# Kernel tuning notes

Hardware: AMD Instinct MI355X
Metric: run time of the kernel (lower is better)

## Reference

```python
import jax, jax.numpy as jnp
import numpy as np

DIM = 384
HEADS = 6
HEAD_DIM = DIM // HEADS
HIDDEN = 4 * DIM
EPS = 1e-5


def layer_norm(x, w, b):
    m = jnp.mean(x, axis=-1, keepdims=True)
    v = jnp.mean((x - m) ** 2, axis=-1, keepdims=True)
    return (x - m) * jax.lax.rsqrt(v + EPS) * w + b


def setup_inputs() -> dict:
    key = jax.random.key(0)
    ks = jax.random.split(key, 8)
    B, N = 2, 4096
    s_in = 1.0 / np.sqrt(DIM)
    s_h = 1.0 / np.sqrt(HIDDEN)
    return {
        "x": jax.random.normal(ks[0], (B, N, DIM), dtype=jnp.float32),
        "qkv_w": jax.random.normal(ks[1], (3 * DIM, DIM), dtype=jnp.float32) * s_in,
        "proj_w": jax.random.normal(ks[2], (DIM, DIM), dtype=jnp.float32) * s_in,
        "proj_b": jnp.zeros((DIM,), dtype=jnp.float32),
        "ln1_w": jnp.ones((DIM,), dtype=jnp.float32),
        "ln1_b": jnp.zeros((DIM,), dtype=jnp.float32),
        "ln2_w": jnp.ones((DIM,), dtype=jnp.float32),
        "ln2_b": jnp.zeros((DIM,), dtype=jnp.float32),
        "fc1_w": jax.random.normal(ks[3], (HIDDEN, DIM), dtype=jnp.float32) * s_in,
        "fc1_b": jnp.zeros((HIDDEN,), dtype=jnp.float32),
        "fc2_w": jax.random.normal(ks[4], (DIM, HIDDEN), dtype=jnp.float32) * s_h,
        "fc2_b": jnp.zeros((DIM,), dtype=jnp.float32),
    }


def reference(x, qkv_w, proj_w, proj_b, ln1_w, ln1_b, ln2_w, ln2_b,
              fc1_w, fc1_b, fc2_w, fc2_b):
    B, N, C = x.shape
    scale = HEAD_DIM ** (-0.5)

    # pre-norm attention
    y = layer_norm(x, ln1_w, ln1_b)
    qkv = (y @ qkv_w.T).reshape(B, N, 3, HEADS, HEAD_DIM)
    qkv = jnp.transpose(qkv, (2, 0, 3, 1, 4))  # [3, B, H, N, D]
    q, k, v = qkv[0], qkv[1], qkv[2]
    attn = jnp.einsum("bhnd,bhmd->bhnm", q, k) * scale  # [B,H,N,N]
    attn = jax.nn.softmax(attn, axis=-1)
    y = jnp.einsum("bhnm,bhmd->bhnd", attn, v)
    y = jnp.transpose(y, (0, 2, 1, 3)).reshape(B, N, C)
    y = y @ proj_w.T + proj_b

    # residual + LN2 + MLP (faithful to source: output = 2 * mlp(ln2(x + y)))
    x = x + y
    x = layer_norm(x, ln2_w, ln2_b)
    h = jax.nn.gelu(x @ fc1_w.T + fc1_b, approximate=False)
    x = h @ fc2_w.T + fc2_b
    x = x + x
    return x
```

## Files before the change

### kernel.cpp

```cpp
#include <hip/hip_runtime.h>
#include <hip/hip_bf16.h>

#define DIM 384
#define HEADS 6
#define HD 64
#define HIDDEN 1536
#define SEQ 4096
#define BATCH 2
#define NTOK (BATCH*SEQ)
#define QKVN (3*DIM)

typedef __attribute__((ext_vector_type(4))) float f32x4;
typedef __attribute__((ext_vector_type(16))) float f32x16;
typedef __attribute__((ext_vector_type(8))) short s16x8;
typedef __attribute__((ext_vector_type(4))) unsigned int u32x4;

__device__ __forceinline__ ushort f2bf(float f) {
    union { float f; unsigned u; } v; v.f = f;
    unsigned r = v.u + 0x7FFF + ((v.u >> 16) & 1);
    return (ushort)(r >> 16);
}
__device__ __forceinline__ float bf2f(ushort b) {
    union { unsigned u; float f; } v; v.u = ((unsigned)b) << 16;
    return v.f;
}
__device__ __forceinline__ unsigned cvtpk(float lo, float hi) {
    unsigned r;
    asm("v_cvt_pk_bf16_f32 %0, %1, %2" : "=v"(r) : "v"(lo), "v"(hi));
    return r;
}
__device__ __forceinline__ void pl32swap(unsigned& a, unsigned& b) {
    asm volatile("v_permlane32_swap_b32 %0, %1" : "+v"(a), "+v"(b));
}
__device__ __forceinline__ void g2l(const ushort* g, ushort* s) {
    __builtin_amdgcn_global_load_lds((const __attribute__((address_space(1))) void*)g,
                                     (__attribute__((address_space(3))) void*)s, 16, 0, 0);
}
__device__ __forceinline__ void blockbar() {
    asm volatile("" ::: "memory");
    __builtin_amdgcn_s_barrier();
    asm volatile("" ::: "memory");
}

__global__ void cvt4_kernel(const float4* __restrict__ s0, ushort* __restrict__ d0, int n0,
                            const float4* __restrict__ s1, ushort* __restrict__ d1, int n1,
                            const float4* __restrict__ s2, ushort* __restrict__ d2, int n2,
                            const float4* __restrict__ s3, ushort* __restrict__ d3, int n3) {
    int i = blockIdx.x * 256 + threadIdx.x;
    const float4* s; ushort* d; int k = i;
    if (i < n0) { s = s0; d = d0; }
    else { k -= n0; if (k < n1) { s = s1; d = d1; }
        else { k -= n1; if (k < n2) { s = s2; d = d2; }
            else { k -= n2; if (k >= n3) return; s = s3; d = d3; } } }
    float4 v = s[k];
    ushort4 o; o.x = f2bf(v.x); o.y = f2bf(v.y); o.z = f2bf(v.z); o.w = f2bf(v.w);
    *(ushort4*)(d + (size_t)k * 4) = o;
}

__global__ __launch_bounds__(256) void ln_kernel(const float* __restrict__ x,
        const float* __restrict__ w, const float* __restrict__ b,
        ushort* __restrict__ y) {
    int l = threadIdx.x & 63;
    int row = blockIdx.x * 4 + (threadIdx.x >> 6);
    const float* xr = x + (size_t)row * DIM;
    float v[6], s = 0.f, s2 = 0.f;
#pragma unroll
    for (int i = 0; i < 6; ++i) { v[i] = xr[l + 64*i]; s += v[i]; s2 += v[i]*v[i]; }
#pragma unroll
    for (int d = 1; d < 64; d <<= 1) { s += __shfl_xor(s, d); s2 += __shfl_xor(s2, d); }
    float mean = s * (1.f/DIM);
    float var  = s2 * (1.f/DIM) - mean*mean;
    float rstd = rsqrtf(var + 1e-5f);
    ushort* yr = y + (size_t)row * DIM;
#pragma unroll
    for (int i = 0; i < 6; ++i) {
        int c = l + 64*i;
        yr[c] = f2bf((v[i]-mean)*rstd*w[c] + b[c]);
    }
}

template<int EPI, int BN>
__global__ __launch_bounds__(256, (BN == 128 ? 3 : 4)) void gemm_kernel(
        const ushort* __restrict__ A, const ushort* __restrict__ W,
        const float* __restrict__ bias, const float* __restrict__ resid,
        void* __restrict__ Cout, int M, int N, int K) {
    __shared__ __align__(16) ushort lds_a[2][64*64];
    __shared__ __align__(16) ushort lds_w[2][BN*64];
    const int t = threadIdx.x, l = t & 63, wid = t >> 6;
    const int lo = l & 15, lg = l >> 4;
    const int m0 = blockIdx.x * 64, n0 = blockIdx.y * BN;
    constexpr int NI = BN / 32;
    constexpr int WW = BN / 32;
    const int wm = (wid & 1) * 32, wn = (wid >> 1) * (BN / 2);
    f32x4 acc[2][NI] = {};

    const int srow8 = l >> 3;
    const int schunk = (l & 7) ^ srow8;
    const ushort* gA[2];
#pragma unroll
    for (int w = 0; w < 2; ++w)
        gA[w] = A + (size_t)(m0 + wid*16 + w*8 + srow8) * K + schunk*8;
    const ushort* gW[WW];
#pragma unroll
    for (int w = 0; w < WW; ++w)
        gW[w] = W + (size_t)(n0 + wid*(8*WW) + w*8 + srow8) * K + schunk*8;

#define STAGE(BUF, K0) do {                                                    \
    _Pragma("unroll")                                                          \
    for (int w = 0; w < 2; ++w)  g2l(gA[w] + (K0), &lds_a[BUF][(wid*16 + w*8)*64]); \
    _Pragma("unroll")                                                          \
    for (int w = 0; w < WW; ++w) g2l(gW[w] + (K0), &lds_w[BUF][(wid*(8*WW) + w*8)*64]); \
} while (0)

#define WAITC do {                                                             \
    if constexpr (BN == 128) asm volatile("s_waitcnt vmcnt(6)" ::: "memory");  \
    else                     asm volatile("s_waitcnt vmcnt(4)" ::: "memory");  \
} while (0)
#define WAIT0 asm volatile("s_waitcnt vmcnt(0)" ::: "memory")

    const int lo7 = lo & 7;
#define COMPUTE(BUF) do {                                                      \
    _Pragma("unroll")                                                          \
    for (int kk = 0; kk < 2; ++kk) {                                           \
        const int ch = ((kk*4 + lg) ^ lo7) * 8;                                \
        s16x8 af[2], bfr[NI];                                                  \
        _Pragma("unroll")                                                      \
        for (int mi = 0; mi < 2; ++mi)                                         \
            af[mi] = *(const s16x8*)&lds_a[BUF][(wm + mi*16 + lo)*64 + ch];    \
        _Pragma("unroll")                                                      \
        for (int ni = 0; ni < NI; ++ni)                                        \
            bfr[ni] = *(const s16x8*)&lds_w[BUF][(wn + ni*16 + lo)*64 + ch];   \
        _Pragma("unroll")                                                      \
        for (int mi = 0; mi < 2; ++mi)                                         \
            _Pragma("unroll")                                                  \
            for (int ni = 0; ni < NI; ++ni)                                    \
                acc[mi][ni] = __builtin_amdgcn_mfma_f32_16x16x32_bf16(af[mi], bfr[ni], acc[mi][ni], 0,0,0); \
    }                                                                          \
} while (0)

    STAGE(0, 0);
    int k0 = 0, remaining = K / 64;
    while (true) {
        if (remaining > 1) { STAGE(1, k0 + 64); WAITC; } else WAIT0;
        blockbar();
        COMPUTE(0);
        blockbar();
        k0 += 64; if (--remaining == 0) break;
        if (remaining > 1) { STAGE(0, k0 + 64); WAITC; } else WAIT0;
        blockbar();
        COMPUTE(1);
        blockbar();
        k0 += 64; if (--remaining == 0) break;
    }
#undef STAGE
#undef WAITC
#undef WAIT0
#undef COMPUTE

#pragma unroll
    for (int mi = 0; mi < 2; ++mi)
#pragma unroll
    for (int ni = 0; ni < NI; ++ni)
#pragma unroll
    for (int r = 0; r < 4; ++r) {
        int row = m0 + wm + mi*16 + lg*4 + r;
        int col = n0 + wn + ni*16 + lo;
        float c = acc[mi][ni][r];
        size_t idx = (size_t)row * N + col;
        if (EPI == 0) {
            ((ushort*)Cout)[idx] = f2bf(c);
        } else if (EPI == 1) {
            ((float*)Cout)[idx] = c + bias[col] + resid[idx];
        } else if (EPI == 2) {
            c += bias[col];
            ((ushort*)Cout)[idx] = f2bf(0.5f * c * (1.f + erff(c * 0.70710678118f)));
        } else {
            ((float*)Cout)[idx] = 2.f * (c + bias[col]);
        }
    }
}

#define PV_STEP(S, MM, CB) do {                                                   \
    unsigned w0 = cvtpk(S[8*MM+0], S[8*MM+1]);                                    \
    unsigned w1 = cvtpk(S[8*MM+2], S[8*MM+3]);                                    \
    unsigned w2 = cvtpk(S[8*MM+4], S[8*MM+5]);                                    \
    unsigned w3 = cvtpk(S[8*MM+6], S[8*MM+7]);                                    \
    pl32swap(w0, w2); pl32swap(w1, w3);                                           \
    u32x4 fw = {w0, w1, w2, w3};                                                  \
    s16x8 pa = __builtin_bit_cast(s16x8, fw);                                     \
    int colb = ((CB) + G*8) ^ swz0;                                               \
    s16x8 vb0 = *(const s16x8*)&lds_v[half][q31][colb];                           \
    s16x8 vb1 = *(const s16x8*)&lds_v[half][32 + q31][colb ^ 32];                 \
    o0 = __builtin_amdgcn_mfma_f32_32x32x16_bf16(pa, vb0, o0, 0,0,0);             \
    o1 = __builtin_amdgcn_mfma_f32_32x32x16_bf16(pa, vb1, o1, 0,0,0);             \
    ol = __builtin_amdgcn_mfma_f32_32x32x16_bf16(pa, vones, ol, 0,0,0);           \
} while (0)

__global__ __launch_bounds__(256, 3) void attn_kernel(const ushort* __restrict__ qkv,
                                                      ushort* __restrict__ out) {
    __shared__ __align__(16) ushort lds_k[2][64][72];
    __shared__ __align__(16) ushort lds_v[2][64][72];
    const int t = threadIdx.x, l = t & 63, wid = t >> 6;
    const int G = l >> 5, q31 = l & 31, half = wid >> 1;
    const int b = blockIdx.y / HEADS, h = blockIdx.y % HEADS;
    const ushort* base = qkv + (size_t)b * SEQ * QKVN + h * HD;
    const int q0 = blockIdx.x * 64 + (wid & 1) * 32;

    const float QSC = 0.1803368801111137f;
    s16x8 qf[4];
#pragma unroll
    for (int dc = 0; dc < 4; ++dc) {
        s16x8 qv = *(const s16x8*)(base + (size_t)(q0 + q31) * QKVN + dc*16 + G*8);
#pragma unroll
        for (int j = 0; j < 8; ++j)
            qv[j] = (short)f2bf(bf2f((ushort)qv[j]) * QSC);
        qf[dc] = qv;
    }
    s16x8 vones;
#pragma unroll
    for (int j = 0; j < 8; ++j) vones[j] = (short)0x3F80;

    f32x16 o0 = {}, o1 = {}, ol = {};

    const int u = t & 127, sa = u >> 3, sc = u & 7;
    const ushort* kbase = base + DIM;
    const ushort* vbase = base + 2*DIM;
    const int key0base = half * (SEQ/2);
    const int swz0 = ((q31 >> 3) & 3) << 3;

    s16x8 kreg[4], vreg[4];
#pragma unroll
    for (int p = 0; p < 4; ++p) {
        kreg[p] = *(const s16x8*)(kbase + (size_t)(key0base + p*16 + sa) * QKVN + sc*8);
        vreg[p] = *(const s16x8*)(vbase + (size_t)(key0base + p*16 + sa) * QKVN + sc*8);
    }

    for (int it = 0; it < 32; ++it) {
        const int key0 = key0base + it*64;
        __syncthreads();
#pragma unroll
        for (int p = 0; p < 4; ++p) {
            *(s16x8*)&lds_k[half][p*16 + sa][sc*8] = kreg[p];
            const int colp = (p*16 + sa) ^ ((sc & 3) << 3) ^ ((sc >> 2) << 5);
#pragma unroll
            for (int j = 0; j < 8; ++j)
                lds_v[half][sc*8 + j][colp] = (ushort)vreg[p][j];
        }
        __syncthreads();
        if (it < 31) {
#pragma unroll
            for (int p = 0; p < 4; ++p) {
                kreg[p] = *(const s16x8*)(kbase + (size_t)(key0 + 64 + p*16 + sa) * QKVN + sc*8);
                vreg[p] = *(const s16x8*)(vbase + (size_t)(key0 + 64 + p*16 + sa) * QKVN + sc*8);
            }
        }

        f32x16 st0 = {}, st1 = {};
        __builtin_amdgcn_s_setprio(1);
#pragma unroll
        for (int dc = 0; dc < 4; ++dc) {
            s16x8 kf0 = *(const s16x8*)&lds_k[half][q31][dc*16 + G*8];
            s16x8 kf1 = *(const s16x8*)&lds_k[half][32 + q31][dc*16 + G*8];
            st0 = __builtin_amdgcn_mfma_f32_32x32x16_bf16(kf0, qf[dc], st0, 0,0,0);
            st1 = __builtin_amdgcn_mfma_f32_32x32x16_bf16(kf1, qf[dc], st1, 0,0,0);
        }
        __builtin_amdgcn_s_setprio(0);

#pragma unroll
        for (int r = 0; r < 16; ++r) {
            st0[r] = exp2f(st0[r]);
            st1[r] = exp2f(st1[r]);
        }

        __builtin_amdgcn_s_setprio(1);
        PV_STEP(st0, 0, 0);
        PV_STEP(st0, 1, 16);
        PV_STEP(st1, 0, 32);
        PV_STEP(st1, 1, 48);
        __builtin_amdgcn_s_setprio(0);
    }

    __syncthreads();
    float* mb = (float*)&lds_k[0][0][0];
    float* ml = (float*)&lds_v[0][0][0];
    if (half == 1) {
#pragma unroll
        for (int r = 0; r < 16; ++r) {
            mb[((wid&1)*2 + 0)*1024 + r*64 + l] = o0[r];
            mb[((wid&1)*2 + 1)*1024 + r*64 + l] = o1[r];
            ml[(wid&1)*1024 + r*64 + l] = ol[r];
        }
    }
    __syncthreads();
    if (half == 0) {
        ushort* ob = out + (size_t)b * SEQ * DIM + h * HD;
#pragma unroll
        for (int r = 0; r < 16; ++r) {
            float invr = 1.0f / (ol[r] + ml[(wid&1)*1024 + r*64 + l]);
            float v0 = (o0[r] + mb[((wid&1)*2 + 0)*1024 + r*64 + l]) * invr;
            float v1 = (o1[r] + mb[((wid&1)*2 + 1)*1024 + r*64 + l]) * invr;
            int qr = (r & 3) + 8*(r >> 2) + 4*G;
            int row = q0 + qr;
            ob[(size_t)row * DIM + q31]      = f2bf(v0);
            ob[(size_t)row * DIM + 32 + q31] = f2bf(v1);
        }
    }
}

extern "C" void kernel_launch(void* const* d_in, const int* in_sizes, int n_in,
                              void* d_out, int out_size, void* d_ws, size_t ws_size,
                              hipStream_t stream) {
    const float* x      = (const float*)d_in[0];
    const float* qkv_w  = (const float*)d_in[1];
    const float* proj_w = (const float*)d_in[2];
    const float* proj_b = (const float*)d_in[3];
    const float* ln1_w  = (const float*)d_in[4];
    const float* ln1_b  = (const float*)d_in[5];
    const float* ln2_w  = (const float*)d_in[6];
    const float* ln2_b  = (const float*)d_in[7];
    const float* fc1_w  = (const float*)d_in[8];
    const float* fc1_b  = (const float*)d_in[9];
    const float* fc2_w  = (const float*)d_in[10];
    const float* fc2_b  = (const float*)d_in[11];
    float* outp = (float*)d_out;

    char* ws = (char*)d_ws;
    size_t off = 0;
    auto alloc = [&](size_t bytes) {
        off = (off + 255) & ~(size_t)255;
        void* p = ws + off;
        off += bytes;
        return p;
    };
    ushort* wq   = (ushort*)alloc((size_t)QKVN * DIM * 2);
    ushort* wp   = (ushort*)alloc((size_t)DIM * DIM * 2);
    ushort* w1   = (ushort*)alloc((size_t)HIDDEN * DIM * 2);
    ushort* w2   = (ushort*)alloc((size_t)DIM * HIDDEN * 2);
    ushort* y1   = (ushort*)alloc((size_t)NTOK * DIM * 2);
    ushort* qkvb = (ushort*)alloc((size_t)NTOK * QKVN * 2);
    ushort* ao   = (ushort*)alloc((size_t)NTOK * DIM * 2);
    float*  res  = (float*) alloc((size_t)NTOK * DIM * 4);
    ushort* y2   = (ushort*)alloc((size_t)NTOK * DIM * 2);
    ushort* hb   = (ushort*)alloc((size_t)NTOK * HIDDEN * 2);

    const int n0 = QKVN*DIM/4, n1 = DIM*DIM/4, n2 = HIDDEN*DIM/4, n3 = DIM*HIDDEN/4;
    cvt4_kernel<<<(n0+n1+n2+n3 + 255)/256, 256, 0, stream>>>(
        (const float4*)qkv_w, wq, n0, (const float4*)proj_w, wp, n1,
        (const float4*)fc1_w, w1, n2, (const float4*)fc2_w, w2, n3);

    ln_kernel<<<NTOK/4, 256, 0, stream>>>(x, ln1_w, ln1_b, y1);
    gemm_kernel<0,128><<<dim3(NTOK/64, QKVN/128), 256, 0, stream>>>(y1, wq, nullptr, nullptr, qkvb, NTOK, QKVN, DIM);
    attn_kernel<<<dim3(SEQ/64, BATCH*HEADS), 256, 0, stream>>>(qkvb, ao);
    gemm_kernel<1,64><<<dim3(NTOK/64, DIM/64), 256, 0, stream>>>(ao, wp, proj_b, x, res, NTOK, DIM, DIM);
    ln_kernel<<<NTOK/4, 256, 0, stream>>>(res, ln2_w, ln2_b, y2);
    gemm_kernel<2,128><<<dim3(NTOK/64, HIDDEN/128), 256, 0, stream>>>(y2, w1, fc1_b, nullptr, hb, NTOK, HIDDEN, DIM);
    gemm_kernel<3,64><<<dim3(NTOK/64, DIM/64), 256, 0, stream>>>(hb, w2, fc2_b, nullptr, outp, NTOK, DIM, HIDDEN);
}
```

Measured before the change: 248.7 us.

## Pre-transpose V in a separate kernel and merge weight cast with LN1

```diff
diff --git a/kernel.cpp b/kernel.cpp
--- a/kernel.cpp
+++ b/kernel.cpp
@@ -42,19 +42,44 @@
     asm volatile("" ::: "memory");
 }
 
-__global__ void cvt4_kernel(const float4* __restrict__ s0, ushort* __restrict__ d0, int n0,
-                            const float4* __restrict__ s1, ushort* __restrict__ d1, int n1,
-                            const float4* __restrict__ s2, ushort* __restrict__ d2, int n2,
-                            const float4* __restrict__ s3, ushort* __restrict__ d3, int n3) {
-    int i = blockIdx.x * 256 + threadIdx.x;
-    const float4* s; ushort* d; int k = i;
-    if (i < n0) { s = s0; d = d0; }
-    else { k -= n0; if (k < n1) { s = s1; d = d1; }
-        else { k -= n1; if (k < n2) { s = s2; d = d2; }
-            else { k -= n2; if (k >= n3) return; s = s3; d = d3; } } }
-    float4 v = s[k];
-    ushort4 o; o.x = f2bf(v.x); o.y = f2bf(v.y); o.z = f2bf(v.z); o.w = f2bf(v.w);
-    *(ushort4*)(d + (size_t)k * 4) = o;
+__global__ __launch_bounds__(256) void prep_kernel(
+        const float4* __restrict__ s0, ushort* __restrict__ d0, int n0,
+        const float4* __restrict__ s1, ushort* __restrict__ d1, int n1,
+        const float4* __restrict__ s2, ushort* __restrict__ d2, int n2,
+        const float4* __restrict__ s3, ushort* __restrict__ d3, int n3,
+        int ncvt,
+        const float* __restrict__ x, const float* __restrict__ lw,
+        const float* __restrict__ lb, ushort* __restrict__ y) {
+    const int bx = blockIdx.x, t = threadIdx.x;
+    if (bx < ncvt) {
+        int i = bx * 256 + t;
+        const float4* s; ushort* d; int k = i;
+        if (i < n0) { s = s0; d = d0; }
+        else { k -= n0; if (k < n1) { s = s1; d = d1; }
+            else { k -= n1; if (k < n2) { s = s2; d = d2; }
+                else { k -= n2; if (k >= n3) return; s = s3; d = d3; } } }
+        float4 v = s[k];
+        ushort4 o; o.x = f2bf(v.x); o.y = f2bf(v.y); o.z = f2bf(v.z); o.w = f2bf(v.w);
+        *(ushort4*)(d + (size_t)k * 4) = o;
+    } else {
+        int l = t & 63;
+        int row = (bx - ncvt) * 4 + (t >> 6);
+        const float* xr = x + (size_t)row * DIM;
+        float v[6], s = 0.f, s2 = 0.f;
+#pragma unroll
+        for (int i = 0; i < 6; ++i) { v[i] = xr[l + 64*i]; s += v[i]; s2 += v[i]*v[i]; }
+#pragma unroll
+        for (int d = 1; d < 64; d <<= 1) { s += __shfl_xor(s, d); s2 += __shfl_xor(s2, d); }
+        float mean = s * (1.f/DIM);
+        float var  = s2 * (1.f/DIM) - mean*mean;
+        float rstd = rsqrtf(var + 1e-5f);
+        ushort* yr = y + (size_t)row * DIM;
+#pragma unroll
+        for (int i = 0; i < 6; ++i) {
+            int c = l + 64*i;
+            yr[c] = f2bf((v[i]-mean)*rstd*lw[c] + lb[c]);
+        }
+    }
 }
 
 __global__ __launch_bounds__(256) void ln_kernel(const float* __restrict__ x,
@@ -76,6 +101,32 @@
     for (int i = 0; i < 6; ++i) {
         int c = l + 64*i;
         yr[c] = f2bf((v[i]-mean)*rstd*w[c] + b[c]);
+    }
+}
+
+__global__ __launch_bounds__(256) void vtrans_kernel(const ushort* __restrict__ qkvb,
+                                                     ushort* __restrict__ vt) {
+    __shared__ __align__(16) ushort lds[64][72];
+    const int t = threadIdx.x;
+    const int key0 = blockIdx.x * 64;
+    const int bh = blockIdx.y;
+    const int b = bh / HEADS, h = bh % HEADS;
+    const ushort* src = qkvb + (size_t)b * SEQ * QKVN + 2*DIM + h*HD;
+    const int ky = t >> 3, c = t & 7;
+#pragma unroll
+    for (int hf = 0; hf < 2; ++hf) {
+        s16x8 v = *(const s16x8*)(src + (size_t)(key0 + hf*32 + ky) * QKVN + c*8);
+        *(s16x8*)&lds[hf*32 + ky][c*8] = v;
+    }
+    __syncthreads();
+    ushort* dst = vt + (size_t)bh * 64 * SEQ + key0;
+#pragma unroll
+    for (int hf = 0; hf < 2; ++hf) {
+        const int d = hf*32 + (t >> 3), kc = t & 7;
+        s16x8 o;
+#pragma unroll
+        for (int j = 0; j < 8; ++j) o[j] = (short)lds[kc*8 + j][d];
+        *(s16x8*)(dst + (size_t)d * SEQ + kc*8) = o;
     }
 }
 
@@ -188,15 +239,16 @@
     pl32swap(w0, w2); pl32swap(w1, w3);                                           \
     u32x4 fw = {w0, w1, w2, w3};                                                  \
     s16x8 pa = __builtin_bit_cast(s16x8, fw);                                     \
-    int colb = ((CB) + G*8) ^ swz0;                                               \
+    int colb = (CB) + G*8;                                                        \
     s16x8 vb0 = *(const s16x8*)&lds_v[half][q31][colb];                           \
-    s16x8 vb1 = *(const s16x8*)&lds_v[half][32 + q31][colb ^ 32];                 \
+    s16x8 vb1 = *(const s16x8*)&lds_v[half][32 + q31][colb];                      \
     o0 = __builtin_amdgcn_mfma_f32_32x32x16_bf16(pa, vb0, o0, 0,0,0);             \
     o1 = __builtin_amdgcn_mfma_f32_32x32x16_bf16(pa, vb1, o1, 0,0,0);             \
     ol = __builtin_amdgcn_mfma_f32_32x32x16_bf16(pa, vones, ol, 0,0,0);           \
 } while (0)
 
 __global__ __launch_bounds__(256, 3) void attn_kernel(const ushort* __restrict__ qkv,
+                                                      const ushort* __restrict__ vt,
                                                       ushort* __restrict__ out) {
     __shared__ __align__(16) ushort lds_k[2][64][72];
     __shared__ __align__(16) ushort lds_v[2][64][72];
@@ -204,6 +256,7 @@
     const int G = l >> 5, q31 = l & 31, half = wid >> 1;
     const int b = blockIdx.y / HEADS, h = blockIdx.y % HEADS;
     const ushort* base = qkv + (size_t)b * SEQ * QKVN + h * HD;
+    const ushort* vtb = vt + (size_t)blockIdx.y * 64 * SEQ;
     const int q0 = blockIdx.x * 64 + (wid & 1) * 32;
 
     const float QSC = 0.1803368801111137f;
@@ -224,15 +277,13 @@
 
     const int u = t & 127, sa = u >> 3, sc = u & 7;
     const ushort* kbase = base + DIM;
-    const ushort* vbase = base + 2*DIM;
     const int key0base = half * (SEQ/2);
-    const int swz0 = ((q31 >> 3) & 3) << 3;
 
     s16x8 kreg[4], vreg[4];
 #pragma unroll
     for (int p = 0; p < 4; ++p) {
         kreg[p] = *(const s16x8*)(kbase + (size_t)(key0base + p*16 + sa) * QKVN + sc*8);
-        vreg[p] = *(const s16x8*)(vbase + (size_t)(key0base + p*16 + sa) * QKVN + sc*8);
+        vreg[p] = *(const s16x8*)(vtb + (size_t)(sa + p*16) * SEQ + key0base + sc*8);
     }
 
     for (int it = 0; it < 32; ++it) {
@@ -241,17 +292,14 @@
 #pragma unroll
         for (int p = 0; p < 4; ++p) {
             *(s16x8*)&lds_k[half][p*16 + sa][sc*8] = kreg[p];
-            const int colp = (p*16 + sa) ^ ((sc & 3) << 3) ^ ((sc >> 2) << 5);
-#pragma unroll
-            for (int j = 0; j < 8; ++j)
-                lds_v[half][sc*8 + j][colp] = (ushort)vreg[p][j];
+            *(s16x8*)&lds_v[half][sa + p*16][sc*8] = vreg[p];
         }
         __syncthreads();
         if (it < 31) {
 #pragma unroll
             for (int p = 0; p < 4; ++p) {
                 kreg[p] = *(const s16x8*)(kbase + (size_t)(key0 + 64 + p*16 + sa) * QKVN + sc*8);
-                vreg[p] = *(const s16x8*)(vbase + (size_t)(key0 + 64 + p*16 + sa) * QKVN + sc*8);
+                vreg[p] = *(const s16x8*)(vtb + (size_t)(sa + p*16) * SEQ + key0 + 64 + sc*8);
             }
         }
 
@@ -338,19 +386,22 @@
     ushort* w2   = (ushort*)alloc((size_t)DIM * HIDDEN * 2);
     ushort* y1   = (ushort*)alloc((size_t)NTOK * DIM * 2);
     ushort* qkvb = (ushort*)alloc((size_t)NTOK * QKVN * 2);
+    ushort* vtb  = (ushort*)alloc((size_t)BATCH * HEADS * HD * SEQ * 2);
     ushort* ao   = (ushort*)alloc((size_t)NTOK * DIM * 2);
     float*  res  = (float*) alloc((size_t)NTOK * DIM * 4);
     ushort* y2   = (ushort*)alloc((size_t)NTOK * DIM * 2);
     ushort* hb   = (ushort*)alloc((size_t)NTOK * HIDDEN * 2);
 
     const int n0 = QKVN*DIM/4, n1 = DIM*DIM/4, n2 = HIDDEN*DIM/4, n3 = DIM*HIDDEN/4;
-    cvt4_kernel<<<(n0+n1+n2+n3 + 255)/256, 256, 0, stream>>>(
+    const int ncvt = (n0+n1+n2+n3 + 255)/256;
+    prep_kernel<<<ncvt + NTOK/4, 256, 0, stream>>>(
         (const float4*)qkv_w, wq, n0, (const float4*)proj_w, wp, n1,
-        (const float4*)fc1_w, w1, n2, (const float4*)fc2_w, w2, n3);
-
-    ln_kernel<<<NTOK/4, 256, 0, stream>>>(x, ln1_w, ln1_b, y1);
+        (const float4*)fc1_w, w1, n2, (const float4*)fc2_w, w2, n3,
+        ncvt, x, ln1_w, ln1_b, y1);
+
     gemm_kernel<0,128><<<dim3(NTOK/64, QKVN/128), 256, 0, stream>>>(y1, wq, nullptr, nullptr, qkvb, NTOK, QKVN, DIM);
-    attn_kernel<<<dim3(SEQ/64, BATCH*HEADS), 256, 0, stream>>>(qkvb, ao);
+    vtrans_kernel<<<dim3(SEQ/64, BATCH*HEADS), 256, 0, stream>>>(qkvb, vtb);
+    attn_kernel<<<dim3(SEQ/64, BATCH*HEADS), 256, 0, stream>>>(qkvb, vtb, ao);
     gemm_kernel<1,64><<<dim3(NTOK/64, DIM/64), 256, 0, stream>>>(ao, wp, proj_b, x, res, NTOK, DIM, DIM);
     ln_kernel<<<NTOK/4, 256, 0, stream>>>(res, ln2_w, ln2_b, y2);
     gemm_kernel<2,128><<<dim3(NTOK/64, HIDDEN/128), 256, 0, stream>>>(y2, w1, fc1_b, nullptr, hb, NTOK, HIDDEN, DIM);
```

Result: no change. 245.9 us (-1.1%).
